# Performance work log

Hardware: AMD Instinct MI355X
Metric: run time of the kernel (lower is better)

## Reference

```python
import jax, jax.numpy as jnp
import numpy as np

N, R, E, H, F = 50000, 6, 32768, 256, 16
NH, HD = 8, 32
EPS_LN = 1e-5

def _ln(x, g, b):
    mu = x.mean(-1, keepdims=True)
    var = ((x - mu) ** 2).mean(-1, keepdims=True)
    return (x - mu) * jax.lax.rsqrt(var + EPS_LN) * g + b

def setup_inputs() -> dict:
    key = jax.random.key(0)
    ks = jax.random.split(key, 32)
    s = lambda i, shape, scale=0.05: jax.random.normal(ks[i], shape, jnp.float32) * scale
    return {
        'x': jax.random.normal(ks[0], (N, H), jnp.float32),
        'edge_index': jax.random.randint(ks[1], (R, 2, E), 0, N, jnp.int32),
        'edge_attr': jax.random.normal(ks[2], (R, E, F), jnp.float32),
        'Wq': s(3, (R, H, H)), 'bq': s(4, (R, H)),
        'Wk': s(5, (R, H + F, H)), 'bk': s(6, (R, H)),
        'Wv': s(7, (R, H + F, H)), 'bv': s(8, (R, H)),
        'prior': jnp.ones((R, NH), jnp.float32),
        'Wm': s(9, (R, H, H)), 'bm': s(10, (R, H)),
        'W_ir1': s(11, (R * H, H)), 'b_ir1': s(12, (H,)),
        'W_ir2': s(13, (H, R)), 'b_ir2': s(14, (R,)),
        'Wmp': s(15, (3, H, H)), 'bmp': s(16, (3, H)),
        'Wa1': s(17, (H, H // 2)), 'ba1': s(18, (H // 2,)),
        'Wa2': s(19, (H // 2, 1)),
        'g_meta': jnp.ones((H,), jnp.float32), 'b_meta': jnp.zeros((H,), jnp.float32),
        'Wc': s(20, (2 * H, H)), 'bc': s(21, (H,)),
        'g_out': jnp.ones((H,), jnp.float32), 'b_out': jnp.zeros((H,), jnp.float32),
    }

def _block(x, edge_index, edge_attr, Wq, bq, Wk, bk, Wv, bv, prior, Wm, bm,
           W_ir1, b_ir1, W_ir2, b_ir2, Wmp, bmp, Wa1, ba1, Wa2, g_meta, b_meta,
           Wc, bc, g_out, b_out):
    def rel_layer(eidx, eattr, wq, bq_, wk, bk_, wv, bv_, pr, wm, bm_):
        src, dst = eidx[0], eidx[1]
        q = x @ wq + bq_                                  # [N,H]
        kv_in = jnp.concatenate([x[src], eattr], -1)      # [E,H+F]
        k = (kv_in @ wk + bk_).reshape(E, NH, HD)
        v = (kv_in @ wv + bv_).reshape(E, NH, HD)
        qe = q[dst].reshape(E, NH, HD)
        scores = (qe * k).sum(-1) / np.sqrt(HD) * pr      # [E,NH]
        m = jax.ops.segment_max(scores, dst, num_segments=N)
        ex = jnp.exp(scores - m[dst])
        denom = jax.ops.segment_sum(ex, dst, num_segments=N)
        w = ex / (denom[dst] + 1e-16)
        wv_flat = (w[..., None] * v).reshape(E, H)
        agg = jax.ops.segment_sum(wv_flat, dst, num_segments=N)  # [N,H]
        return jax.nn.gelu(agg @ wm + bm_, approximate=False)

    rel_out = jax.vmap(rel_layer)(edge_index, edge_attr, Wq, bq, Wk, bk, Wv, bv,
                                  prior, Wm, bm)          # [R,N,H]

    all_rel = jnp.transpose(rel_out, (1, 0, 2)).reshape(N, R * H)
    h = jax.nn.gelu(all_rel @ W_ir1 + b_ir1, approximate=False)
    inter_w = jax.nn.softmax(h @ W_ir2 + b_ir2, axis=-1)  # [N,R]
    inter_agg = jnp.einsum('nr,rnh->nh', inter_w, rel_out)

    # meta-paths: 0=entangle(ENTANGLE=2,SWAP=3) 1=control(CONTROL=4,ROTATION=0) 2=local(PAULI=1,TEMPORAL=5)
    paths = jnp.stack([rel_out[2] + rel_out[3], rel_out[4] + rel_out[0],
                       rel_out[1] + rel_out[5]], axis=1)  # [N,3,H]
    stacked = jnp.einsum('nph,phk->npk', paths, Wmp) + bmp
    attn = jax.nn.softmax((jnp.tanh(stacked @ Wa1 + ba1) @ Wa2).squeeze(-1), axis=1)
    meta = _ln((attn[..., None] * stacked).sum(1), g_meta, b_meta)

    combined = jax.nn.gelu(jnp.concatenate([inter_agg, meta], -1) @ Wc + bc,
                           approximate=False)
    return _ln(x + combined, g_out, b_out)

def reference(x, edge_index, edge_attr, Wq, bq, Wk, bk, Wv, bv, prior, Wm, bm,
              W_ir1, b_ir1, W_ir2, b_ir2, Wmp, bmp, Wa1, ba1, Wa2, g_meta, b_meta,
              Wc, bc, g_out, b_out):
    return _block(x, edge_index, edge_attr, Wq, bq, Wk, bk, Wv, bv, prior, Wm, bm,
                  W_ir1, b_ir1, W_ir2, b_ir2, Wmp, bmp, Wa1, ba1, Wa2,
                  g_meta, b_meta, Wc, bc, g_out, b_out)
```

## Files before the change

kernel.cpp:

```cpp
#include <hip/hip_runtime.h>
#include <hip/hip_bf16.h>

typedef __hip_bfloat16 bf16;
typedef __attribute__((ext_vector_type(8))) short short8;
typedef __attribute__((ext_vector_type(4))) float f32x4;

#define NN 50000
#define RR 6
#define EE 32768
#define HH 256
#define FF 16
#define NHEAD 8
#define KVP 320

struct __align__(8) bf16x4 { bf16 v[4]; };

__device__ __forceinline__ float b2f(bf16 v) { return __bfloat162float(v); }
__device__ __forceinline__ bf16 f2b(float v) { return __float2bfloat16(v); }
__device__ __forceinline__ short f2s(float f) { bf16 b = f2b(f); return __builtin_bit_cast(short, b); }
__device__ __forceinline__ float s2f(short s) { return b2f(__builtin_bit_cast(bf16, s)); }
__device__ __forceinline__ float gelu_f(float x) { return 0.5f * x * (1.0f + erff(x * 0.7071067811865476f)); }
__device__ __forceinline__ unsigned fkey(float f) { unsigned u = __float_as_uint(f); return (u & 0x80000000u) ? ~u : (u | 0x80000000u); }
__device__ __forceinline__ float fdec(unsigned k) { unsigned u = (k & 0x80000000u) ? (k & 0x7fffffffu) : ~k; return __uint_as_float(u); }

__device__ __forceinline__ void gl2lds16(const void* g, void* l) {
  __builtin_amdgcn_global_load_lds(
      (const __attribute__((address_space(1))) unsigned int*)g,
      (__attribute__((address_space(3))) unsigned int*)l, 16, 0, 0);
}

__global__ void zero_k(uint4* __restrict__ p, int n16)
{
  const uint4 z = make_uint4(0u, 0u, 0u, 0u);
  for (int i = blockIdx.x * blockDim.x + threadIdx.x; i < n16; i += gridDim.x * blockDim.x)
    p[i] = z;
}

__global__ void cvt_k(const float* __restrict__ in, bf16* __restrict__ out, int n4)
{
  const int i = blockIdx.x * 256 + threadIdx.x;
  if (i >= n4) return;
  const float4 f = ((const float4*)in)[i];
  bf16x4 o; o.v[0] = f2b(f.x); o.v[1] = f2b(f.y); o.v[2] = f2b(f.z); o.v[3] = f2b(f.w);
  ((bf16x4*)out)[i] = o;
}

__global__ void tconv_k(const float* __restrict__ in, bf16* __restrict__ out,
                        int K, int NC, int Kp, long izs, long ozs)
{
  __shared__ float t[32][33];
  in  += (size_t)blockIdx.z * izs;
  out += (size_t)blockIdx.z * ozs;
  const int kb = blockIdx.x * 32, nb = blockIdx.y * 32;
  const int tx = threadIdx.x & 31, ty = threadIdx.x >> 5;
  for (int i = ty; i < 32; i += 8) {
    const int k = kb + i, n = nb + tx;
    t[i][tx] = (k < K && n < NC) ? in[(size_t)k * NC + n] : 0.f;
  }
  __syncthreads();
  for (int i = ty; i < 32; i += 8) {
    const int n = nb + i, k = kb + tx;
    if (n < NC && k < Kp) out[(size_t)n * Kp + k] = f2b(t[tx][i]);
  }
}

__global__ void bkv_k(const float* __restrict__ bk, const float* __restrict__ bv,
                      float* __restrict__ bkv)
{
  const int i = blockIdx.x * 256 + threadIdx.x;
  if (i >= RR * 512) return;
  const int r = i >> 9, c = i & 511;
  bkv[i] = (c < 256) ? bk[r * 256 + c] : bv[r * 256 + (c - 256)];
}

__global__ void copyslot_k(const bf16* __restrict__ tmp, bf16* __restrict__ slot)
{
  const int i = blockIdx.x * 256 + threadIdx.x;
  if (i >= NN * 32) return;
  const int n = i >> 5, c = (i & 31) * 8;
  *(short8*)(slot + (size_t)n * 1536 + c) = *(const short8*)(tmp + (size_t)n * 256 + c);
}

template<int ASRC, int ACT, bool LOGITS, typename TO>
__global__ __launch_bounds__(256) void mm_k(
    const void* __restrict__ Av, const bf16* __restrict__ A2, int lda,
    const int* __restrict__ src, const float* __restrict__ eattr,
    const bf16* __restrict__ Bt, const float* __restrict__ bias,
    const float* __restrict__ wa2, TO* __restrict__ C, int ldc,
    float* __restrict__ logits, int M, int K)
{
  __shared__ short lA[128 * 64];
  __shared__ short lB[128 * 64];
  const int tid = threadIdx.x;
  const int w = tid >> 6, l = tid & 63;
  const int col0 = blockIdx.x << 7;
  const int row0 = blockIdx.y << 7;
  const bf16* Ab = (const bf16*)Av;
  float* lg = logits;
  if constexpr (LOGITS) {
    const int slots3[3] = {2, 4, 1};
    Ab = (const bf16*)Av + slots3[blockIdx.z] * 256;
    lg = logits + (size_t)blockIdx.z * M;
  }
  const int wm = (w >> 1) << 6, wn = (w & 1) << 6;
  const int lane15 = l & 15, kq = l >> 4;

  f32x4 acc[4][4] = {};

  for (int k0 = 0; k0 < K; k0 += 64) {
#pragma unroll
    for (int i = 0; i < 4; ++i) {
      const int idx = (w * 4 + i) * 64 + l;
      const int row = idx >> 3, cg = idx & 7;
      const int scg = cg ^ (row & 7);
      const int r = min(row0 + row, M - 1);
      const int kc = k0 + scg * 8;
      if constexpr (ASRC == 0) {
        gl2lds16(Ab + (size_t)r * lda + kc, &lA[idx * 8]);
      } else if constexpr (ASRC == 1) {
        const float* p = (const float*)Av + (size_t)r * lda + kc;
        const float4 f0 = *(const float4*)p;
        const float4 f1 = *(const float4*)(p + 4);
        short8 s;
        s[0] = f2s(f0.x); s[1] = f2s(f0.y); s[2] = f2s(f0.z); s[3] = f2s(f0.w);
        s[4] = f2s(f1.x); s[5] = f2s(f1.y); s[6] = f2s(f1.z); s[7] = f2s(f1.w);
        *(short8*)&lA[idx * 8] = s;
      } else if constexpr (ASRC == 2) {
        const short8 u = *(const short8*)((const bf16*)Av + (size_t)r * lda + kc);
        const short8 v2 = *(const short8*)(A2 + (size_t)r * lda + kc);
        short8 s;
#pragma unroll
        for (int j = 0; j < 8; ++j) s[j] = f2s(s2f(u[j]) + s2f(v2[j]));
        *(short8*)&lA[idx * 8] = s;
      } else {
        short8 s;
        if (kc < HH) {
          s = *(const short8*)((const bf16*)Av + (size_t)src[r] * HH + kc);
        } else if (kc < HH + FF) {
          const float* p = eattr + (size_t)r * FF + (kc - HH);
          const float4 f0 = *(const float4*)p;
          const float4 f1 = *(const float4*)(p + 4);
          s[0] = f2s(f0.x); s[1] = f2s(f0.y); s[2] = f2s(f0.z); s[3] = f2s(f0.w);
          s[4] = f2s(f1.x); s[5] = f2s(f1.y); s[6] = f2s(f1.z); s[7] = f2s(f1.w);
        } else {
#pragma unroll
          for (int j = 0; j < 8; ++j) s[j] = 0;
        }
        *(short8*)&lA[idx * 8] = s;
      }
    }
#pragma unroll
    for (int i = 0; i < 4; ++i) {
      const int idx = (w * 4 + i) * 64 + l;
      const int row = idx >> 3, cg = idx & 7;
      const int scg = cg ^ (row & 7);
      gl2lds16(Bt + (size_t)(col0 + row) * K + k0 + scg * 8, &lB[idx * 8]);
    }
    __syncthreads();
#pragma unroll
    for (int kk = 0; kk < 64; kk += 32) {
      short8 af[4], bfr[4];
#pragma unroll
      for (int t = 0; t < 4; ++t) {
        const int ra = wm + t * 16 + lane15;
        const int ca = ((kk >> 3) + kq) ^ (ra & 7);
        af[t] = *(const short8*)&lA[ra * 64 + ca * 8];
        const int rb = wn + t * 16 + lane15;
        const int cb = ((kk >> 3) + kq) ^ (rb & 7);
        bfr[t] = *(const short8*)&lB[rb * 64 + cb * 8];
      }
#pragma unroll
      for (int ti = 0; ti < 4; ++ti)
#pragma unroll
        for (int tj = 0; tj < 4; ++tj)
          acc[ti][tj] = __builtin_amdgcn_mfma_f32_16x16x32_bf16(af[ti], bfr[tj], acc[ti][tj], 0, 0, 0);
    }
    __syncthreads();
  }

  if constexpr (!LOGITS) {
#pragma unroll
    for (int ti = 0; ti < 4; ++ti) {
#pragma unroll
      for (int reg = 0; reg < 4; ++reg) {
        const int row = row0 + wm + ti * 16 + kq * 4 + reg;
        if (row >= M) continue;
#pragma unroll
        for (int tj = 0; tj < 4; ++tj) {
          const int col = col0 + wn + tj * 16 + lane15;
          float v = acc[ti][tj][reg] + bias[col];
          if constexpr (ACT == 1) v = gelu_f(v);
          if constexpr (sizeof(TO) == 2) C[(size_t)row * ldc + col] = (TO)f2b(v);
          else                           C[(size_t)row * ldc + col] = (TO)v;
        }
      }
    }
  } else {
#pragma unroll
    for (int ti = 0; ti < 4; ++ti) {
#pragma unroll
      for (int reg = 0; reg < 4; ++reg) {
        float part = 0.f;
#pragma unroll
        for (int tj = 0; tj < 4; ++tj) {
          const int col = col0 + wn + tj * 16 + lane15;
          part += tanhf(acc[ti][tj][reg] + bias[col]) * wa2[col];
        }
#pragma unroll
        for (int off = 8; off > 0; off >>= 1) part += __shfl_xor(part, off, 64);
        const int row = row0 + wm + ti * 16 + kq * 4 + reg;
        if (lane15 == 0 && row < M) atomicAdd(&lg[row], part);
      }
    }
  }
}

__global__ void scores_k(const bf16* __restrict__ q, const bf16* __restrict__ kv,
                         const int* __restrict__ dst_idx, const float* __restrict__ prior_r,
                         float* __restrict__ scores, unsigned* __restrict__ mkey)
{
  const int e = blockIdx.x, t = threadIdx.x;
  const int dst = dst_idx[e];
  float p = b2f(q[(size_t)dst * 1536 + t]) * b2f(kv[(size_t)e * 512 + t]);
#pragma unroll
  for (int off = 16; off > 0; off >>= 1) p += __shfl_down(p, off, 32);
  const int h = t >> 5;
  if ((t & 31) == 0) {
    const float s = p * 0.1767766952966369f * prior_r[h];
    scores[e * NHEAD + h] = s;
    atomicMax(&mkey[dst * NHEAD + h], fkey(s));
  }
}

__global__ void expden_k(const float* __restrict__ scores, const int* __restrict__ dst_idx,
                         const unsigned* __restrict__ mkey, float* __restrict__ ex,
                         float* __restrict__ denom)
{
  const int idx = blockIdx.x * 256 + threadIdx.x;
  if (idx >= EE * NHEAD) return;
  const int e = idx >> 3, h = idx & 7;
  const int dst = dst_idx[e];
  const float m = fdec(mkey[dst * NHEAD + h]);
  const float v = expf(scores[idx] - m);
  ex[idx] = v;
  atomicAdd(&denom[dst * NHEAD + h], v);
}

__global__ void agg_k(const float* __restrict__ ex, const float* __restrict__ denom,
                      const bf16* __restrict__ kv, const int* __restrict__ dst_idx,
                      float* __restrict__ agg)
{
  const int e = blockIdx.x, t = threadIdx.x, h = t >> 5;
  const int dst = dst_idx[e];
  const float w = ex[e * NHEAD + h] / (denom[dst * NHEAD + h] + 1e-16f);
  atomicAdd(&agg[(size_t)dst * HH + t], w * b2f(kv[(size_t)e * 512 + 256 + t]));
}

__global__ void interw_k(const bf16* __restrict__ h, const float* __restrict__ W2,
                         const float* __restrict__ b2, float* __restrict__ interw)
{
  const int wv = threadIdx.x >> 6, ln = threadIdx.x & 63;
  const int n = blockIdx.x * 4 + wv;
  if (n >= NN) return;
  float a[6] = {0.f, 0.f, 0.f, 0.f, 0.f, 0.f};
#pragma unroll
  for (int kq = 0; kq < 4; ++kq) {
    const int k = ln + (kq << 6);
    const float hv = b2f(h[(size_t)n * HH + k]);
#pragma unroll
    for (int j = 0; j < 6; ++j) a[j] += hv * W2[k * 6 + j];
  }
#pragma unroll
  for (int j = 0; j < 6; ++j) {
#pragma unroll
    for (int off = 32; off > 0; off >>= 1) a[j] += __shfl_down(a[j], off, 64);
  }
  if (ln == 0) {
    float lg[6], e[6], mx = -1e30f, s = 0.f;
#pragma unroll
    for (int j = 0; j < 6; ++j) { lg[j] = a[j] + b2[j]; mx = fmaxf(mx, lg[j]); }
#pragma unroll
    for (int j = 0; j < 6; ++j) { e[j] = expf(lg[j] - mx); s += e[j]; }
    const float inv = 1.0f / s;
#pragma unroll
    for (int j = 0; j < 6; ++j) interw[(size_t)n * 6 + j] = e[j] * inv;
  }
}

__global__ void interagg_k(const float* __restrict__ interw, const bf16* __restrict__ rel_cat,
                           bf16* __restrict__ comb)
{
  const int n = blockIdx.x, t = threadIdx.x;
  float acc = 0.f;
#pragma unroll
  for (int r = 0; r < 6; ++r)
    acc += interw[(size_t)n * 6 + r] * b2f(rel_cat[(size_t)n * 1536 + r * 256 + t]);
  comb[(size_t)n * 512 + t] = f2b(acc);
}

__global__ void metafinal_k(const float* __restrict__ logits, const bf16* __restrict__ rel_cat,
                            const float* __restrict__ gmeta, const float* __restrict__ bmeta,
                            bf16* __restrict__ comb)
{
  const int wv = threadIdx.x >> 6, ln = threadIdx.x & 63;
  const int n = blockIdx.x * 4 + wv;
  if (n >= NN) return;
  const float l0 = logits[n], l1 = logits[NN + n], l2 = logits[2 * NN + n];
  const float mx = fmaxf(l0, fmaxf(l1, l2));
  const float e0 = expf(l0 - mx), e1 = expf(l1 - mx), e2 = expf(l2 - mx);
  const float inv = 1.0f / (e0 + e1 + e2);
  const float a0 = e0 * inv, a1 = e1 * inv, a2 = e2 * inv;
  const size_t base = (size_t)n * 1536;
  float pre[4], s = 0.f, s2 = 0.f;
#pragma unroll
  for (int q4 = 0; q4 < 4; ++q4) {
    const int j = ln + (q4 << 6);
    const float v = a0 * b2f(rel_cat[base + 2 * 256 + j])
                  + a1 * b2f(rel_cat[base + 4 * 256 + j])
                  + a2 * b2f(rel_cat[base + 1 * 256 + j]);
    pre[q4] = v; s += v; s2 += v * v;
  }
#pragma unroll
  for (int off = 32; off > 0; off >>= 1) { s += __shfl_down(s, off, 64); s2 += __shfl_down(s2, off, 64); }
  s = __shfl(s, 0, 64); s2 = __shfl(s2, 0, 64);
  const float mu = s * (1.0f / 256.0f);
  const float var = s2 * (1.0f / 256.0f) - mu * mu;
  const float rs = rsqrtf(var + 1e-5f);
#pragma unroll
  for (int q4 = 0; q4 < 4; ++q4) {
    const int j = ln + (q4 << 6);
    comb[(size_t)n * 512 + 256 + j] = f2b((pre[q4] - mu) * rs * gmeta[j] + bmeta[j]);
  }
}

__global__ void final_k(const float* __restrict__ x, const float* __restrict__ combined,
                        const float* __restrict__ g, const float* __restrict__ b,
                        float* __restrict__ out)
{
  __shared__ float sred[8];
  const int n = blockIdx.x, t = threadIdx.x;
  const float v = x[(size_t)n * HH + t] + combined[(size_t)n * HH + t];
  float s = v, s2 = v * v;
#pragma unroll
  for (int off = 32; off > 0; off >>= 1) { s += __shfl_down(s, off, 64); s2 += __shfl_down(s2, off, 64); }
  const int wv = t >> 6;
  if ((t & 63) == 0) { sred[wv] = s; sred[4 + wv] = s2; }
  __syncthreads();
  const float st = sred[0] + sred[1] + sred[2] + sred[3];
  const float st2 = sred[4] + sred[5] + sred[6] + sred[7];
  const float mu = st * (1.0f / 256.0f);
  const float var = st2 * (1.0f / 256.0f) - mu * mu;
  const float rs = rsqrtf(var + 1e-5f);
  out[(size_t)n * HH + t] = (v - mu) * rs * g[t] + b[t];
}

extern "C" void kernel_launch(void* const* d_in, const int* in_sizes, int n_in,
                              void* d_out, int out_size, void* d_ws, size_t ws_size,
                              hipStream_t stream)
{
  const float* x      = (const float*)d_in[0];
  const int*   eidx   = (const int*)d_in[1];
  const float* eattr  = (const float*)d_in[2];
  const float* Wq     = (const float*)d_in[3];
  const float* bq     = (const float*)d_in[4];
  const float* Wk     = (const float*)d_in[5];
  const float* bk     = (const float*)d_in[6];
  const float* Wv     = (const float*)d_in[7];
  const float* bv     = (const float*)d_in[8];
  const float* prior  = (const float*)d_in[9];
  const float* Wm     = (const float*)d_in[10];
  const float* bm     = (const float*)d_in[11];
  const float* W_ir1  = (const float*)d_in[12];
  const float* b_ir1  = (const float*)d_in[13];
  const float* W_ir2  = (const float*)d_in[14];
  const float* b_ir2  = (const float*)d_in[15];
  const float* Wmp    = (const float*)d_in[16];
  const float* bmp    = (const float*)d_in[17];
  const float* Wa1    = (const float*)d_in[18];
  const float* ba1    = (const float*)d_in[19];
  const float* Wa2    = (const float*)d_in[20];
  const float* g_meta = (const float*)d_in[21];
  const float* b_meta = (const float*)d_in[22];
  const float* Wc     = (const float*)d_in[23];
  const float* bc     = (const float*)d_in[24];
  const float* g_out  = (const float*)d_in[25];
  const float* b_out  = (const float*)d_in[26];
  float* out = (float*)d_out;

  char* ws = (char*)d_ws;
  bf16* rel_cat = (bf16*)ws;
  char* W0 = ws + 153600000;
  bf16*  Wqt   = (bf16*)(W0 + 0);
  bf16*  Wkvt  = (bf16*)(W0 + 786432);
  bf16*  Wmt   = (bf16*)(W0 + 2752512);
  bf16*  Wir1t = (bf16*)(W0 + 3538944);
  bf16*  Wct   = (bf16*)(W0 + 4325376);
  bf16*  Wmpt  = (bf16*)(W0 + 4587520);
  bf16*  Wa1t  = (bf16*)(W0 + 4980736);
  float* bkv   = (float*)(W0 + 5046272);
  char* region = ws + 158658560;
  bf16*     kvbuf = (bf16*)(region + 0);
  float*    sc    = (float*)(region + 33554432);
  float*    exb   = (float*)(region + 34603008);
  unsigned* mkey  = (unsigned*)(region + 35651584);
  float*    denom = (float*)(region + 37251584);
  bf16*     xb    = (bf16*)(region + 38851584);
  float*    agg   = out;
  bf16*  hbuf     = (bf16*)(region + 0);
  float* interw   = (float*)(region + 33554432);
  bf16*  tmp      = (bf16*)(region + 25600000);
  float* logits   = (float*)(region + 51200000);
  bf16*  comb     = (bf16*)out;
  float* combined = (float*)(region + 0);

  const dim3 gN(2, 391);
  const dim3 gQ(12, 391);
  const dim3 gKV(4, 256);
  const dim3 gL(1, 391, 3);

  tconv_k<<<dim3(8, 8, 6), 256, 0, stream>>>(Wq, Wqt, 256, 256, 256, 256 * 256, 256 * 256);
  tconv_k<<<dim3(10, 8, 6), 256, 0, stream>>>(Wk, Wkvt, 272, 256, 320, 272 * 256, 512 * 320);
  tconv_k<<<dim3(10, 8, 6), 256, 0, stream>>>(Wv, Wkvt + 256 * 320, 272, 256, 320, 272 * 256, 512 * 320);
  tconv_k<<<dim3(8, 8, 6), 256, 0, stream>>>(Wm, Wmt, 256, 256, 256, 256 * 256, 256 * 256);
  tconv_k<<<dim3(48, 8, 1), 256, 0, stream>>>(W_ir1, Wir1t, 1536, 256, 1536, 0, 0);
  tconv_k<<<dim3(16, 8, 1), 256, 0, stream>>>(Wc, Wct, 512, 256, 512, 0, 0);
  tconv_k<<<dim3(8, 8, 3), 256, 0, stream>>>(Wmp, Wmpt, 256, 256, 256, 256 * 256, 256 * 256);
  tconv_k<<<dim3(8, 4, 1), 256, 0, stream>>>(Wa1, Wa1t, 256, 128, 256, 0, 0);
  bkv_k<<<12, 256, 0, stream>>>(bk, bv, bkv);
  cvt_k<<<(NN * 64 + 255) / 256, 256, 0, stream>>>(x, xb, NN * 64);

  mm_k<0, 0, false, bf16><<<gQ, 256, 0, stream>>>(
      xb, nullptr, 256, nullptr, nullptr,
      Wqt, bq, nullptr, rel_cat, 1536, nullptr, NN, 256);

  for (int r = 0; r < RR; ++r) {
    const int* src = eidx + (size_t)r * 2 * EE;
    const int* dst = src + EE;
    const float* ea = eattr + (size_t)r * EE * FF;
    zero_k<<<391, 256, 0, stream>>>((uint4*)mkey, (2 * NN * NHEAD * 4) / 16);
    zero_k<<<2048, 256, 0, stream>>>((uint4*)agg, (NN * HH * 4) / 16);
    mm_k<3, 0, false, bf16><<<gKV, 256, 0, stream>>>(
        xb, nullptr, 0, src, ea,
        Wkvt + (size_t)r * 512 * KVP, bkv + r * 512, nullptr, kvbuf, 512, nullptr, EE, KVP);
    scores_k<<<EE, 256, 0, stream>>>(rel_cat + r * 256, kvbuf, dst, prior + r * NHEAD, sc, mkey);
    expden_k<<<(EE * NHEAD + 255) / 256, 256, 0, stream>>>(sc, dst, mkey, exb, denom);
    agg_k<<<EE, 256, 0, stream>>>(exb, denom, kvbuf, dst, agg);
    mm_k<1, 1, false, bf16><<<gN, 256, 0, stream>>>(
        agg, nullptr, 256, nullptr, nullptr,
        Wmt + (size_t)r * 256 * 256, bm + r * HH, nullptr,
        rel_cat + r * 256, 1536, nullptr, NN, 256);
  }

  mm_k<0, 1, false, bf16><<<gN, 256, 0, stream>>>(
      rel_cat, nullptr, 1536, nullptr, nullptr,
      Wir1t, b_ir1, nullptr, hbuf, 256, nullptr, NN, 1536);
  interw_k<<<(NN + 3) / 4, 256, 0, stream>>>(hbuf, W_ir2, b_ir2, interw);
  interagg_k<<<NN, 256, 0, stream>>>(interw, rel_cat, comb);

  const int r1[3] = {2, 4, 1};
  const int r2[3] = {3, 0, 5};
  for (int p = 0; p < 3; ++p) {
    mm_k<2, 0, false, bf16><<<gN, 256, 0, stream>>>(
        rel_cat + r1[p] * 256, rel_cat + r2[p] * 256, 1536, nullptr, nullptr,
        Wmpt + (size_t)p * 256 * 256, bmp + p * 256, nullptr, tmp, 256, nullptr, NN, 256);
    copyslot_k<<<(NN * 32 + 255) / 256, 256, 0, stream>>>(tmp, rel_cat + r1[p] * 256);
  }
  zero_k<<<147, 256, 0, stream>>>((uint4*)logits, (3 * NN * 4) / 16);
  mm_k<0, 0, true, bf16><<<gL, 256, 0, stream>>>(
      rel_cat, nullptr, 1536, nullptr, nullptr,
      Wa1t, ba1, Wa2, (bf16*)nullptr, 0, logits, NN, 256);
  metafinal_k<<<(NN + 3) / 4, 256, 0, stream>>>(logits, rel_cat, g_meta, b_meta, comb);

  mm_k<0, 1, false, float><<<gN, 256, 0, stream>>>(
      comb, nullptr, 512, nullptr, nullptr,
      Wct, bc, nullptr, combined, 256, nullptr, NN, 512);
  final_k<<<NN, 256, 0, stream>>>(x, combined, g_out, b_out, out);
}
```

Baseline: 1.582 ms.

## Replace LDS-tiled GEMM with direct-load register GEMM and in-place meta-path writes

Replaces the shared-memory tiled 128x128 GEMM with a kernel where each wave loads its A and B fragments straight from global memory into registers. Each wave computes a 32x64 tile, block shapes are configurable, and occupancy hints are added. The meta-path GEMM now writes its output directly into the rel_cat slot, which removes the temporary buffer and the copy kernel. This drops the LDS staging and barriers, but cross-wave reuse then depends on cache, so global and L2 traffic may rise.

```diff
diff --git a/kernel.cpp b/kernel.cpp
--- a/kernel.cpp
+++ b/kernel.cpp
@@ -22,12 +22,6 @@
 __device__ __forceinline__ float gelu_f(float x) { return 0.5f * x * (1.0f + erff(x * 0.7071067811865476f)); }
 __device__ __forceinline__ unsigned fkey(float f) { unsigned u = __float_as_uint(f); return (u & 0x80000000u) ? ~u : (u | 0x80000000u); }
 __device__ __forceinline__ float fdec(unsigned k) { unsigned u = (k & 0x80000000u) ? (k & 0x7fffffffu) : ~k; return __uint_as_float(u); }
-
-__device__ __forceinline__ void gl2lds16(const void* g, void* l) {
-  __builtin_amdgcn_global_load_lds(
-      (const __attribute__((address_space(1))) unsigned int*)g,
-      (__attribute__((address_space(3))) unsigned int*)l, 16, 0, 0);
-}
 
 __global__ void zero_k(uint4* __restrict__ p, int n16)
 {
@@ -73,28 +67,21 @@
   bkv[i] = (c < 256) ? bk[r * 256 + c] : bv[r * 256 + (c - 256)];
 }
 
-__global__ void copyslot_k(const bf16* __restrict__ tmp, bf16* __restrict__ slot)
-{
-  const int i = blockIdx.x * 256 + threadIdx.x;
-  if (i >= NN * 32) return;
-  const int n = i >> 5, c = (i & 31) * 8;
-  *(short8*)(slot + (size_t)n * 1536 + c) = *(const short8*)(tmp + (size_t)n * 256 + c);
-}
-
-template<int ASRC, int ACT, bool LOGITS, typename TO>
-__global__ __launch_bounds__(256) void mm_k(
+template<int ASRC, int ACT, bool LOGITS, int BCW, typename TO>
+__global__ __launch_bounds__(256, 4) void mmd_k(
     const void* __restrict__ Av, const bf16* __restrict__ A2, int lda,
     const int* __restrict__ src, const float* __restrict__ eattr,
     const bf16* __restrict__ Bt, const float* __restrict__ bias,
     const float* __restrict__ wa2, TO* __restrict__ C, int ldc,
     float* __restrict__ logits, int M, int K)
 {
-  __shared__ short lA[128 * 64];
-  __shared__ short lB[128 * 64];
+  constexpr int BROWS = (4 / BCW) * 32;
   const int tid = threadIdx.x;
   const int w = tid >> 6, l = tid & 63;
-  const int col0 = blockIdx.x << 7;
-  const int row0 = blockIdx.y << 7;
+  const int lane15 = l & 15, kq = l >> 4;
+  const int wr = w / BCW, wc = w % BCW;
+  const int row0 = blockIdx.y * BROWS + wr * 32;
+  const int col0 = blockIdx.x * (BCW * 64) + wc * 64;
   const bf16* Ab = (const bf16*)Av;
   float* lg = logits;
   if constexpr (LOGITS) {
@@ -102,92 +89,80 @@
     Ab = (const bf16*)Av + slots3[blockIdx.z] * 256;
     lg = logits + (size_t)blockIdx.z * M;
   }
-  const int wm = (w >> 1) << 6, wn = (w & 1) << 6;
-  const int lane15 = l & 15, kq = l >> 4;
-
-  f32x4 acc[4][4] = {};
+  int ra[2], se[2] = {0, 0};
+#pragma unroll
+  for (int ti = 0; ti < 2; ++ti) {
+    ra[ti] = min(row0 + ti * 16 + lane15, M - 1);
+    if constexpr (ASRC == 3) se[ti] = src[ra[ti]];
+  }
+  f32x4 acc[2][4] = {};
 
   for (int k0 = 0; k0 < K; k0 += 64) {
 #pragma unroll
-    for (int i = 0; i < 4; ++i) {
-      const int idx = (w * 4 + i) * 64 + l;
-      const int row = idx >> 3, cg = idx & 7;
-      const int scg = cg ^ (row & 7);
-      const int r = min(row0 + row, M - 1);
-      const int kc = k0 + scg * 8;
-      if constexpr (ASRC == 0) {
-        gl2lds16(Ab + (size_t)r * lda + kc, &lA[idx * 8]);
-      } else if constexpr (ASRC == 1) {
-        const float* p = (const float*)Av + (size_t)r * lda + kc;
-        const float4 f0 = *(const float4*)p;
-        const float4 f1 = *(const float4*)(p + 4);
-        short8 s;
-        s[0] = f2s(f0.x); s[1] = f2s(f0.y); s[2] = f2s(f0.z); s[3] = f2s(f0.w);
-        s[4] = f2s(f1.x); s[5] = f2s(f1.y); s[6] = f2s(f1.z); s[7] = f2s(f1.w);
-        *(short8*)&lA[idx * 8] = s;
-      } else if constexpr (ASRC == 2) {
-        const short8 u = *(const short8*)((const bf16*)Av + (size_t)r * lda + kc);
-        const short8 v2 = *(const short8*)(A2 + (size_t)r * lda + kc);
-        short8 s;
-#pragma unroll
-        for (int j = 0; j < 8; ++j) s[j] = f2s(s2f(u[j]) + s2f(v2[j]));
-        *(short8*)&lA[idx * 8] = s;
-      } else {
-        short8 s;
-        if (kc < HH) {
-          s = *(const short8*)((const bf16*)Av + (size_t)src[r] * HH + kc);
-        } else if (kc < HH + FF) {
-          const float* p = eattr + (size_t)r * FF + (kc - HH);
+    for (int kk = 0; kk < 64; kk += 32) {
+      const int kb = k0 + kk + kq * 8;
+      short8 af[2], bfr[4];
+#pragma unroll
+      for (int ti = 0; ti < 2; ++ti) {
+        if constexpr (ASRC == 0) {
+          af[ti] = *(const short8*)(Ab + (size_t)ra[ti] * lda + kb);
+        } else if constexpr (ASRC == 1) {
+          const float* p = (const float*)Av + (size_t)ra[ti] * lda + kb;
           const float4 f0 = *(const float4*)p;
           const float4 f1 = *(const float4*)(p + 4);
+          short8 s;
           s[0] = f2s(f0.x); s[1] = f2s(f0.y); s[2] = f2s(f0.z); s[3] = f2s(f0.w);
           s[4] = f2s(f1.x); s[5] = f2s(f1.y); s[6] = f2s(f1.z); s[7] = f2s(f1.w);
+          af[ti] = s;
+        } else if constexpr (ASRC == 2) {
+          const short8 u  = *(const short8*)((const bf16*)Av + (size_t)ra[ti] * lda + kb);
+          const short8 v2 = *(const short8*)(A2 + (size_t)ra[ti] * lda + kb);
+          short8 s;
+#pragma unroll
+          for (int j = 0; j < 8; ++j) s[j] = f2s(s2f(u[j]) + s2f(v2[j]));
+          af[ti] = s;
         } else {
-#pragma unroll
-          for (int j = 0; j < 8; ++j) s[j] = 0;
+          if (kb < HH) {
+            af[ti] = *(const short8*)((const bf16*)Av + (size_t)se[ti] * HH + kb);
+          } else if (kb < HH + FF) {
+            const float* p = eattr + (size_t)ra[ti] * FF + (kb - HH);
+            const float4 f0 = *(const float4*)p;
+            const float4 f1 = *(const float4*)(p + 4);
+            short8 s;
+            s[0] = f2s(f0.x); s[1] = f2s(f0.y); s[2] = f2s(f0.z); s[3] = f2s(f0.w);
+            s[4] = f2s(f1.x); s[5] = f2s(f1.y); s[6] = f2s(f1.z); s[7] = f2s(f1.w);
+            af[ti] = s;
+          } else {
+            short8 s;
+#pragma unroll
+            for (int j = 0; j < 8; ++j) s[j] = 0;
+            af[ti] = s;
+          }
         }
-        *(short8*)&lA[idx * 8] = s;
       }
-    }
-#pragma unroll
-    for (int i = 0; i < 4; ++i) {
-      const int idx = (w * 4 + i) * 64 + l;
-      const int row = idx >> 3, cg = idx & 7;
-      const int scg = cg ^ (row & 7);
-      gl2lds16(Bt + (size_t)(col0 + row) * K + k0 + scg * 8, &lB[idx * 8]);
-    }
-    __syncthreads();
-#pragma unroll
-    for (int kk = 0; kk < 64; kk += 32) {
-      short8 af[4], bfr[4];
-#pragma unroll
-      for (int t = 0; t < 4; ++t) {
-        const int ra = wm + t * 16 + lane15;
-        const int ca = ((kk >> 3) + kq) ^ (ra & 7);
-        af[t] = *(const short8*)&lA[ra * 64 + ca * 8];
-        const int rb = wn + t * 16 + lane15;
-        const int cb = ((kk >> 3) + kq) ^ (rb & 7);
-        bfr[t] = *(const short8*)&lB[rb * 64 + cb * 8];
-      }
-#pragma unroll
-      for (int ti = 0; ti < 4; ++ti)
+#pragma unroll
+      for (int tj = 0; tj < 4; ++tj)
+        bfr[tj] = *(const short8*)(Bt + (size_t)(col0 + tj * 16 + lane15) * K + kb);
+#pragma unroll
+      for (int ti = 0; ti < 2; ++ti)
 #pragma unroll
         for (int tj = 0; tj < 4; ++tj)
           acc[ti][tj] = __builtin_amdgcn_mfma_f32_16x16x32_bf16(af[ti], bfr[tj], acc[ti][tj], 0, 0, 0);
     }
-    __syncthreads();
-  }
+  }
+
+  __syncthreads();
 
   if constexpr (!LOGITS) {
 #pragma unroll
-    for (int ti = 0; ti < 4; ++ti) {
+    for (int ti = 0; ti < 2; ++ti) {
 #pragma unroll
       for (int reg = 0; reg < 4; ++reg) {
-        const int row = row0 + wm + ti * 16 + kq * 4 + reg;
+        const int row = row0 + ti * 16 + kq * 4 + reg;
         if (row >= M) continue;
 #pragma unroll
         for (int tj = 0; tj < 4; ++tj) {
-          const int col = col0 + wn + tj * 16 + lane15;
+          const int col = col0 + tj * 16 + lane15;
           float v = acc[ti][tj][reg] + bias[col];
           if constexpr (ACT == 1) v = gelu_f(v);
           if constexpr (sizeof(TO) == 2) C[(size_t)row * ldc + col] = (TO)f2b(v);
@@ -197,18 +172,18 @@
     }
   } else {
 #pragma unroll
-    for (int ti = 0; ti < 4; ++ti) {
+    for (int ti = 0; ti < 2; ++ti) {
 #pragma unroll
       for (int reg = 0; reg < 4; ++reg) {
         float part = 0.f;
 #pragma unroll
         for (int tj = 0; tj < 4; ++tj) {
-          const int col = col0 + wn + tj * 16 + lane15;
+          const int col = col0 + tj * 16 + lane15;
           part += tanhf(acc[ti][tj][reg] + bias[col]) * wa2[col];
         }
 #pragma unroll
         for (int off = 8; off > 0; off >>= 1) part += __shfl_xor(part, off, 64);
-        const int row = row0 + wm + ti * 16 + kq * 4 + reg;
+        const int row = row0 + ti * 16 + kq * 4 + reg;
         if (lane15 == 0 && row < M) atomicAdd(&lg[row], part);
       }
     }
@@ -408,15 +383,15 @@
   float*    agg   = out;
   bf16*  hbuf     = (bf16*)(region + 0);
   float* interw   = (float*)(region + 33554432);
-  bf16*  tmp      = (bf16*)(region + 25600000);
   float* logits   = (float*)(region + 51200000);
   bf16*  comb     = (bf16*)out;
   float* combined = (float*)(region + 0);
 
-  const dim3 gN(2, 391);
-  const dim3 gQ(12, 391);
-  const dim3 gKV(4, 256);
-  const dim3 gL(1, 391, 3);
+  const dim3 gQ(12, 782);
+  const dim3 gN2(2, 782);
+  const dim3 gKV(4, 512);
+  const dim3 gMP(1, 1563);
+  const dim3 gL(1, 782, 3);
 
   tconv_k<<<dim3(8, 8, 6), 256, 0, stream>>>(Wq, Wqt, 256, 256, 256, 256 * 256, 256 * 256);
   tconv_k<<<dim3(10, 8, 6), 256, 0, stream>>>(Wk, Wkvt, 272, 256, 320, 272 * 256, 512 * 320);
@@ -429,7 +404,7 @@
   bkv_k<<<12, 256, 0, stream>>>(bk, bv, bkv);
   cvt_k<<<(NN * 64 + 255) / 256, 256, 0, stream>>>(x, xb, NN * 64);
 
-  mm_k<0, 0, false, bf16><<<gQ, 256, 0, stream>>>(
+  mmd_k<0, 0, false, 2, bf16><<<gQ, 256, 0, stream>>>(
       xb, nullptr, 256, nullptr, nullptr,
       Wqt, bq, nullptr, rel_cat, 1536, nullptr, NN, 256);
 
@@ -439,19 +414,19 @@
     const float* ea = eattr + (size_t)r * EE * FF;
     zero_k<<<391, 256, 0, stream>>>((uint4*)mkey, (2 * NN * NHEAD * 4) / 16);
     zero_k<<<2048, 256, 0, stream>>>((uint4*)agg, (NN * HH * 4) / 16);
-    mm_k<3, 0, false, bf16><<<gKV, 256, 0, stream>>>(
+    mmd_k<3, 0, false, 2, bf16><<<gKV, 256, 0, stream>>>(
         xb, nullptr, 0, src, ea,
         Wkvt + (size_t)r * 512 * KVP, bkv + r * 512, nullptr, kvbuf, 512, nullptr, EE, KVP);
     scores_k<<<EE, 256, 0, stream>>>(rel_cat + r * 256, kvbuf, dst, prior + r * NHEAD, sc, mkey);
     expden_k<<<(EE * NHEAD + 255) / 256, 256, 0, stream>>>(sc, dst, mkey, exb, denom);
     agg_k<<<EE, 256, 0, stream>>>(exb, denom, kvbuf, dst, agg);
-    mm_k<1, 1, false, bf16><<<gN, 256, 0, stream>>>(
+    mmd_k<1, 1, false, 2, bf16><<<gN2, 256, 0, stream>>>(
         agg, nullptr, 256, nullptr, nullptr,
         Wmt + (size_t)r * 256 * 256, bm + r * HH, nullptr,
         rel_cat + r * 256, 1536, nullptr, NN, 256);
   }
 
-  mm_k<0, 1, false, bf16><<<gN, 256, 0, stream>>>(
+  mmd_k<0, 1, false, 2, bf16><<<gN2, 256, 0, stream>>>(
       rel_cat, nullptr, 1536, nullptr, nullptr,
       Wir1t, b_ir1, nullptr, hbuf, 256, nullptr, NN, 1536);
   interw_k<<<(NN + 3) / 4, 256, 0, stream>>>(hbuf, W_ir2, b_ir2, interw);
@@ -460,18 +435,18 @@
   const int r1[3] = {2, 4, 1};
   const int r2[3] = {3, 0, 5};
   for (int p = 0; p < 3; ++p) {
-    mm_k<2, 0, false, bf16><<<gN, 256, 0, stream>>>(
+    mmd_k<2, 0, false, 4, bf16><<<gMP, 256, 0, stream>>>(
         rel_cat + r1[p] * 256, rel_cat + r2[p] * 256, 1536, nullptr, nullptr,
-        Wmpt + (size_t)p * 256 * 256, bmp + p * 256, nullptr, tmp, 256, nullptr, NN, 256);
-    copyslot_k<<<(NN * 32 + 255) / 256, 256, 0, stream>>>(tmp, rel_cat + r1[p] * 256);
+        Wmpt + (size_t)p * 256 * 256, bmp + p * 256, nullptr,
+        rel_cat + r1[p] * 256, 1536, nullptr, NN, 256);
   }
   zero_k<<<147, 256, 0, stream>>>((uint4*)logits, (3 * NN * 4) / 16);
-  mm_k<0, 0, true, bf16><<<gL, 256, 0, stream>>>(
+  mmd_k<0, 0, true, 2, bf16><<<gL, 256, 0, stream>>>(
       rel_cat, nullptr, 1536, nullptr, nullptr,
       Wa1t, ba1, Wa2, (bf16*)nullptr, 0, logits, NN, 256);
   metafinal_k<<<(NN + 3) / 4, 256, 0, stream>>>(logits, rel_cat, g_meta, b_meta, comb);
 
-  mm_k<0, 1, false, float><<<gN, 256, 0, stream>>>(
+  mmd_k<0, 1, false, 2, float><<<gN2, 256, 0, stream>>>(
       comb, nullptr, 512, nullptr, nullptr,
       Wct, bc, nullptr, combined, 256, nullptr, NN, 512);
   final_k<<<NN, 256, 0, stream>>>(x, combined, g_out, b_out, out);
```

Measured after the change: 2.384 ms. +50.6%, slower.
